# Optimization experiments

Measured on AMD Instinct MI355X. Metric: run time of the kernel, lower is better.

The kernel has to match this reference:

```python
import jax, jax.numpy as jnp
import numpy as np

P = 16; D = 256; NH = 8; L = 4; E = 8; K = 2; B = 32; IMG = 224; NC = 1000; FF = 4 * D
N = (IMG // P) ** 2  # 196 patches
HD = D // NH  # head dim
EPS = 1e-5


def setup_inputs():
    key = jax.random.key(0)
    ks = iter(jax.random.split(key, 16))
    s = 0.02  # init scale keeps softmax/logits well-conditioned
    rn = lambda shape: jax.random.normal(next(ks), shape, jnp.float32) * s
    return dict(
        x=jax.random.normal(next(ks), (B, 3, IMG, IMG), jnp.float32),
        patch_w=rn((3 * P * P, D)), patch_b=jnp.zeros((D,), jnp.float32),
        cls_token=rn((1, 1, D)), pos_embed=rn((1, N + 1, D)),
        router_w=rn((L, D, E)), router_b=jnp.zeros((L, E), jnp.float32),
        ln1_g=jnp.ones((L, E, D), jnp.float32), ln1_b=jnp.zeros((L, E, D), jnp.float32),
        qkv_w=rn((L, E, D, 3 * D)), qkv_b=jnp.zeros((L, E, 3 * D), jnp.float32),
        proj_w=rn((L, E, D, D)), proj_b=jnp.zeros((L, E, D), jnp.float32),
        ln2_g=jnp.ones((L, E, D), jnp.float32), ln2_b=jnp.zeros((L, E, D), jnp.float32),
        fc1_w=rn((L, E, D, FF)), fc1_b=jnp.zeros((L, E, FF), jnp.float32),
        fc2_w=rn((L, E, FF, D)), fc2_b=jnp.zeros((L, E, D), jnp.float32),
        norm_g=jnp.ones((D,), jnp.float32), norm_b=jnp.zeros((D,), jnp.float32),
        head_w=rn((D, NC)), head_b=jnp.zeros((NC,), jnp.float32),
    )


def _ln(x, g, b):
    m = x.mean(-1, keepdims=True)
    v = ((x - m) ** 2).mean(-1, keepdims=True)
    return (x - m) * jax.lax.rsqrt(v + EPS) * g + b


def _block(x, g1, b1, wqkv, bqkv, wp, bp, g2, b2, w1, bias1, w2, bias2):
    # standard ViT block: LN -> MHA -> residual, LN -> MLP(GELU) -> residual
    bsz, S, _ = x.shape
    h = _ln(x, g1, b1)
    qkv = (h @ wqkv + bqkv).reshape(bsz, S, 3, NH, HD)
    q, k, v = qkv[:, :, 0], qkv[:, :, 1], qkv[:, :, 2]  # [B,S,NH,HD]
    scores = jnp.einsum('bqhd,bkhd->bhqk', q, k) / np.float32(np.sqrt(HD))
    attn = jax.nn.softmax(scores, axis=-1)
    o = jnp.einsum('bhqk,bkhd->bqhd', attn, v).reshape(bsz, S, D)
    x = x + o @ wp + bp
    h2 = _ln(x, g2, b2)
    x = x + jax.nn.gelu(h2 @ w1 + bias1, approximate=False) @ w2 + bias2
    return x


def _moe_layer(x, rw, rb, g1, b1, wqkv, bqkv, wp, bp, g2, b2, w1, bias1, w2, bias2):
    probs = jax.nn.softmax(x @ rw + rb, axis=-1)            # [B,S,E]
    topv, topi = jax.lax.top_k(probs, K)                    # [B,S,K]
    topv = topv / topv.sum(-1, keepdims=True)
    # dense all-expert compute (faithful to source), vmapped over experts
    eo = jax.vmap(_block, in_axes=(None,) + (0,) * 12)(
        x, g1, b1, wqkv, bqkv, wp, bp, g2, b2, w1, bias1, w2, bias2)  # [E,B,S,D]
    eo = jnp.moveaxis(eo, 0, 2)                             # [B,S,E,D]
    sel = jnp.take_along_axis(eo, topi[..., None], axis=2)  # [B,S,K,D]
    return (sel * topv[..., None]).sum(axis=2)


def reference(x, patch_w, patch_b, cls_token, pos_embed, router_w, router_b,
              ln1_g, ln1_b, qkv_w, qkv_b, proj_w, proj_b, ln2_g, ln2_b,
              fc1_w, fc1_b, fc2_w, fc2_b, norm_g, norm_b, head_w, head_b):
    bsz = x.shape[0]
    g = IMG // P
    # patch embed: stride==kernel conv == patch extraction + matmul
    patches = x.reshape(bsz, 3, g, P, g, P).transpose(0, 2, 4, 1, 3, 5).reshape(bsz, N, 3 * P * P)
    h = patches @ patch_w + patch_b                          # [B,N,D]
    cls = jnp.broadcast_to(cls_token, (bsz, 1, D))
    h = jnp.concatenate([cls, h], axis=1) + pos_embed        # [B,N+1,D]
    for l in range(L):
        h = _moe_layer(h, router_w[l], router_b[l], ln1_g[l], ln1_b[l],
                       qkv_w[l], qkv_b[l], proj_w[l], proj_b[l], ln2_g[l], ln2_b[l],
                       fc1_w[l], fc1_b[l], fc2_w[l], fc2_b[l])
    h = _ln(h, norm_g, norm_b)
    return h[:, 0] @ head_w + head_b                         # [B,NC]
```

## Files before the change

kernel.cpp:

```cpp
#include <hip/hip_runtime.h>
#include <math.h>

#define SEQ 197
#define BATCH 32
#define DIM 256
#define NHEAD 8
#define HDIM 32
#define NEXP 8
#define NLAYER 4
#define FFDIM 1024
#define NCLS 1000
#define NPATCH 196
#define TOK (BATCH * SEQ)
#define CAP 13120
#define YB 99
#define YB128 50
#define KT 64

__device__ __forceinline__ void gload16(const float* g, float* l) {
  __builtin_amdgcn_global_load_lds(
      (const __attribute__((address_space(1))) void*)g,
      (__attribute__((address_space(3))) void*)l, 16, 0, 0);
}

__global__ __launch_bounds__(256) void k_im2col(const float* __restrict__ x,
                                                float* __restrict__ Apat) {
  int idx = blockIdx.x * 256 + threadIdx.x;
  if (idx >= BATCH * NPATCH * 768) return;
  int cpp = idx % 768;
  int m = idx / 768;
  int n = m % NPATCH;
  int b = m / NPATCH;
  int c = cpp >> 8;
  int py = (cpp >> 4) & 15;
  int px = cpp & 15;
  int gy = n / 14, gx = n % 14;
  Apat[idx] = x[(((size_t)b * 3 + c) * 224 + gy * 16 + py) * 224 + gx * 16 + px];
}

__global__ __launch_bounds__(256) void k_foldw(const float* __restrict__ qw,
                                               const float* __restrict__ g1,
                                               float* __restrict__ w4) {
  size_t idx = (size_t)blockIdx.x * 256 + threadIdx.x;
  if (idx >= (size_t)32 * 256 * 768) return;
  size_t kn = idx % (256 * 768);
  int le = (int)(idx / (256 * 768));
  int k = (int)(kn / 768);
  w4[idx] = qw[idx] * g1[le * 256 + k];
}

__global__ __launch_bounds__(256) void k_foldb(const float* __restrict__ qw,
                                               const float* __restrict__ qb,
                                               const float* __restrict__ b1,
                                               float* __restrict__ b4) {
  int le = blockIdx.y;
  int col = blockIdx.x * 256 + threadIdx.x;
  const float* w = qw + (size_t)le * 256 * 768 + col;
  const float* lb = b1 + (size_t)le * 256;
  float acc = 0.f;
  for (int k = 0; k < 256; ++k) acc = fmaf(lb[k], w[(size_t)k * 768], acc);
  b4[(size_t)le * 768 + col] = acc + qb[(size_t)le * 768 + col];
}

__global__ __launch_bounds__(256) void k_gemm_t(
    const float* __restrict__ A, const float* __restrict__ W,
    const float* __restrict__ bias, const float* __restrict__ R,
    const float* __restrict__ X2, const float* __restrict__ PW,
    const int* __restrict__ ptok, const int* __restrict__ off_e,
    const int* __restrict__ cnt_e, float* __restrict__ out, int M, int N,
    int K, int Ktot, int ksplit, int Wld, int wcol, int bstride, int ebase,
    int mode, int flags) {
  __shared__ float As[2][16][68];
  __shared__ float Bs[2][16][64];
  int gx = gridDim.x, gy = gridDim.y;
  int nwg = gx * gy * gridDim.z;
  int lin = blockIdx.x + gx * (blockIdx.y + gy * blockIdx.z);
  int q8 = nwg >> 3, r8 = nwg & 7;
  int xcd = lin & 7, jj0 = lin >> 3;
  int nlin = (xcd < r8 ? xcd * (q8 + 1) : r8 * (q8 + 1) + (xcd - r8) * q8) + jj0;
  int bx = nlin % gx;
  int t1 = nlin / gx;
  int by = t1 % gy;
  int bzf = t1 / gy;
  int kz = bzf % ksplit;
  int ez = bzf / ksplit;

  int e = ebase + ez;
  bool seg = (flags & 1) != 0;
  bool first = (kz == 0);
  int rows = seg ? cnt_e[e] : M;
  int row0 = by * 64;
  if (row0 >= rows) return;
  int col0 = bx * 64;
  int kbase = kz * K;
  int tid = threadIdx.x;
  int base = seg ? off_e[e] : 0;
  const float* Wp = W + (size_t)e * Ktot * Wld + wcol;
  const float* bp = bias + (size_t)e * bstride + wcol;

  int rr = tid >> 2, kq = (tid & 3) * 4;
  int r = row0 + rr;
  bool val = r < rows;
  int rc = val ? r : rows - 1;
  int gr0 = base + rc;
  int arow = seg ? ((flags & 2) ? ptok[gr0] : gr0) : rc;
  const float* aptr = A + (size_t)arow * Ktot + kbase + kq;
  float msk = val ? 1.f : 0.f;
  int wv = tid >> 6, lane = tid & 63;
  const float* bsrc = Wp + (size_t)(kbase + 4 * wv + (lane >> 4)) * Wld +
                      col0 + (lane & 15) * 4;

  gload16(bsrc, &Bs[0][4 * wv][0]);
  {
    float4 av = *(const float4*)aptr;
    As[0][kq + 0][rr] = av.x * msk;
    As[0][kq + 1][rr] = av.y * msk;
    As[0][kq + 2][rr] = av.z * msk;
    As[0][kq + 3][rr] = av.w * msk;
  }
  __syncthreads();

  int tx = tid & 15, ty = tid >> 4;
  float acc[4][4] = {};
  int cur = 0;
  for (int k0 = 0; k0 < K; k0 += 16) {
    int nb = cur ^ 1;
    bool more = (k0 + 16) < K;
    float4 av;
    if (more) {
      av = *(const float4*)(aptr + k0 + 16);
      gload16(bsrc + (size_t)(k0 + 16) * Wld, &Bs[nb][4 * wv][0]);
    }
#pragma unroll
    for (int k = 0; k < 16; ++k) {
      float4 a = *(const float4*)&As[cur][k][ty * 4];
      float4 b = *(const float4*)&Bs[cur][k][tx * 4];
      float aa[4] = {a.x, a.y, a.z, a.w};
      float bb[4] = {b.x, b.y, b.z, b.w};
#pragma unroll
      for (int i = 0; i < 4; ++i)
#pragma unroll
        for (int j = 0; j < 4; ++j) acc[i][j] = fmaf(aa[i], bb[j], acc[i][j]);
    }
    if (more) {
      As[nb][kq + 0][rr] = av.x * msk;
      As[nb][kq + 1][rr] = av.y * msk;
      As[nb][kq + 2][rr] = av.z * msk;
      As[nb][kq + 3][rr] = av.w * msk;
    }
    __syncthreads();
    cur = nb;
  }
#pragma unroll
  for (int i = 0; i < 4; ++i) {
    int rrow = row0 + ty * 4 + i;
    if (rrow >= rows) continue;
    int gr = base + rrow;
#pragma unroll
    for (int j = 0; j < 4; ++j) {
      int col = col0 + tx * 4 + j;
      float v = acc[i][j] + (first ? bp[col] : 0.f);
      if (mode == 0) {
        size_t orow = seg ? (size_t)gr : (size_t)bzf * M + rrow;
        out[orow * N + col] = v;
      } else if (mode == 1) {
        int t = ptok[gr];
        out[(size_t)gr * N + col] = v + R[(size_t)t * N + col];
      } else if (mode == 2) {
        out[(size_t)gr * N + col] =
            0.5f * v * (1.f + erff(v * 0.70710678118654752f));
      } else {
        int t = ptok[gr];
        float x2v = first ? X2[(size_t)gr * N + col] : 0.f;
        atomicAdd(&out[(size_t)t * N + col], PW[gr] * (x2v + v));
      }
    }
  }
}

__global__ __launch_bounds__(256) void k_gemm16(
    const float* __restrict__ A, const float* __restrict__ W,
    const float* __restrict__ bias, const float* __restrict__ R,
    const float* __restrict__ X2, const float* __restrict__ PW,
    const int* __restrict__ ptok, const int* __restrict__ off_e,
    const int* __restrict__ cnt_e, float* __restrict__ out, int M, int N,
    int K, int Wld, int wcol, int bstride, int ebase, int mode, int flags) {
  __shared__ float As[2][128][16];
  __shared__ float Bs[2][16][128];
  int gx = gridDim.x, gy = gridDim.y;
  int nwg = gx * gy * gridDim.z;
  int lin = blockIdx.x + gx * (blockIdx.y + gy * blockIdx.z);
  int q8 = nwg >> 3, r8 = nwg & 7;
  int xcd = lin & 7, jj0 = lin >> 3;
  int nlin = (xcd < r8 ? xcd * (q8 + 1) : r8 * (q8 + 1) + (xcd - r8) * q8) + jj0;
  int bx = nlin % gx;
  int t1 = nlin / gx;
  int by = t1 % gy;
  int bz = t1 / gy;

  int e = ebase + bz;
  bool seg = (flags & 1) != 0;
  int rows = seg ? cnt_e[e] : M;
  int row0 = by * 128;
  if (row0 >= rows) return;
  int col0 = bx * 128;
  int tid = threadIdx.x;
  int wv = tid >> 6, lane = tid & 63;
  int base = seg ? off_e[e] : 0;
  const float* Wp = W + (size_t)e * K * Wld + wcol;
  const float* bp = bias + (size_t)e * bstride + wcol;

  const float* pA0;
  const float* pA1;
  {
    int l4 = lane >> 2, lk = (lane & 3) * 4;
#pragma unroll
    for (int c = 0; c < 2; ++c) {
      int r = row0 + wv * 32 + c * 16 + l4;
      int rc = r < rows ? r : rows - 1;
      int gr0 = base + rc;
      int arow = seg ? ((flags & 2) ? ptok[gr0] : gr0) : rc;
      const float* p = A + (size_t)arow * K + lk;
      if (c == 0) pA0 = p; else pA1 = p;
    }
  }
  const float* pB = Wp + (size_t)(4 * wv + (lane >> 5)) * Wld + col0 +
                    (lane & 31) * 4;

  gload16(pA0, &As[0][wv * 32][0]);
  gload16(pA1, &As[0][wv * 32 + 16][0]);
  gload16(pB, &Bs[0][4 * wv][0]);
  gload16(pB + (size_t)2 * Wld, &Bs[0][4 * wv + 2][0]);
  __syncthreads();

  int tx = tid & 15, ty = tid >> 4;
  float acc0[8][4] = {};
  float acc1[8][4] = {};
  int cur = 0;
  for (int k0 = 0; k0 < K; k0 += 16) {
    int nb = cur ^ 1;
    bool more = (k0 + 16) < K;
    if (more) {
      gload16(pA0 + k0 + 16, &As[nb][wv * 32][0]);
      gload16(pA1 + k0 + 16, &As[nb][wv * 32 + 16][0]);
      gload16(pB + (size_t)(k0 + 16) * Wld, &Bs[nb][4 * wv][0]);
      gload16(pB + (size_t)(k0 + 18) * Wld, &Bs[nb][4 * wv + 2][0]);
    }
#pragma unroll
    for (int k4 = 0; k4 < 4; ++k4) {
      float a[8][4];
#pragma unroll
      for (int i = 0; i < 8; ++i) {
        float4 t = *(const float4*)&As[cur][ty + 16 * i][k4 * 4];
        a[i][0] = t.x;
        a[i][1] = t.y;
        a[i][2] = t.z;
        a[i][3] = t.w;
      }
#pragma unroll
      for (int kk = 0; kk < 4; ++kk) {
        float4 b0 = *(const float4*)&Bs[cur][k4 * 4 + kk][tx * 4];
        float4 b1 = *(const float4*)&Bs[cur][k4 * 4 + kk][64 + tx * 4];
        float b0a[4] = {b0.x, b0.y, b0.z, b0.w};
        float b1a[4] = {b1.x, b1.y, b1.z, b1.w};
#pragma unroll
        for (int i = 0; i < 8; ++i) {
          float av = a[i][kk];
#pragma unroll
          for (int j = 0; j < 4; ++j) {
            acc0[i][j] = fmaf(av, b0a[j], acc0[i][j]);
            acc1[i][j] = fmaf(av, b1a[j], acc1[i][j]);
          }
        }
      }
    }
    __syncthreads();
    cur = nb;
  }
#pragma unroll
  for (int i = 0; i < 8; ++i) {
    int rrow = row0 + ty + 16 * i;
    if (rrow >= rows) continue;
    int gr = base + rrow;
#pragma unroll
    for (int c = 0; c < 2; ++c) {
#pragma unroll
      for (int j = 0; j < 4; ++j) {
        int col = col0 + c * 64 + tx * 4 + j;
        float v = (c ? acc1[i][j] : acc0[i][j]) + bp[col];
        if (mode == 0) {
          size_t orow = seg ? (size_t)gr : (size_t)bz * M + rrow;
          out[orow * N + col] = v;
        } else if (mode == 1) {
          int t = ptok[gr];
          out[(size_t)gr * N + col] = v + R[(size_t)t * N + col];
        } else if (mode == 2) {
          out[(size_t)gr * N + col] =
              0.5f * v * (1.f + erff(v * 0.70710678118654752f));
        } else {
          int t = ptok[gr];
          atomicAdd(&out[(size_t)t * N + col],
                    PW[gr] * (X2[(size_t)gr * N + col] + v));
        }
      }
    }
  }
}

__global__ __launch_bounds__(256) void k_assemble(const float* __restrict__ tmp,
                                                  const float* __restrict__ cls,
                                                  const float* __restrict__ pos,
                                                  float* __restrict__ h) {
  int idx = blockIdx.x * 256 + threadIdx.x;
  if (idx >= TOK * DIM) return;
  int d = idx & 255;
  int t = idx >> 8;
  int s = t % SEQ;
  int b = t / SEQ;
  float v = (s == 0) ? cls[d] : tmp[((size_t)b * NPATCH + s - 1) * DIM + d];
  h[idx] = v + pos[s * DIM + d];
}

__global__ __launch_bounds__(64) void k_router(
    const float* __restrict__ h, const float* __restrict__ rw,
    const float* __restrict__ rb, int* __restrict__ cnt_eb,
    int* __restrict__ tmp_s, float* __restrict__ tmp_w) {
  int t = blockIdx.x;
  int lane = threadIdx.x;
  float hv[4];
  const float* hp = h + (size_t)t * DIM + lane * 4;
#pragma unroll
  for (int i = 0; i < 4; i++) hv[i] = hp[i];
  float lg[8];
#pragma unroll
  for (int e = 0; e < 8; e++) {
    float p = 0.f;
#pragma unroll
    for (int i = 0; i < 4; i++) p = fmaf(hv[i], rw[(lane * 4 + i) * 8 + e], p);
#pragma unroll
    for (int off = 32; off; off >>= 1) p += __shfl_down(p, off);
    lg[e] = p;
  }
  if (lane == 0) {
#pragma unroll
    for (int e = 0; e < 8; e++) lg[e] += rb[e];
    float mx = lg[0];
#pragma unroll
    for (int e = 1; e < 8; e++) mx = fmaxf(mx, lg[e]);
    float pr[8];
#pragma unroll
    for (int e = 0; e < 8; e++) pr[e] = expf(lg[e] - mx);
    int i0 = 0;
#pragma unroll
    for (int e = 1; e < 8; e++)
      if (pr[e] > pr[i0]) i0 = e;
    int i1 = -1;
#pragma unroll
    for (int e = 0; e < 8; e++)
      if (e != i0 && (i1 < 0 || pr[e] > pr[i1])) i1 = e;
    float wsum = pr[i0] + pr[i1];
    int b = t / SEQ, s = t - b * SEQ;
    int eb0 = i0 * 32 + b;
    int p0 = atomicAdd(&cnt_eb[eb0], 1);
    tmp_s[eb0 * SEQ + p0] = s;
    tmp_w[eb0 * SEQ + p0] = pr[i0] / wsum;
    int eb1 = i1 * 32 + b;
    int p1 = atomicAdd(&cnt_eb[eb1], 1);
    tmp_s[eb1 * SEQ + p1] = s;
    tmp_w[eb1 * SEQ + p1] = pr[i1] / wsum;
  }
}

__global__ __launch_bounds__(64) void k_scan(const int* __restrict__ cnt_eb,
                                             int* __restrict__ off_eb,
                                             int* __restrict__ off_e,
                                             int* __restrict__ cnt_e) {
  if (threadIdx.x == 0 && blockIdx.x == 0) {
    int g = 0;
    for (int e = 0; e < 8; e++) {
      off_e[e] = g;
      int ce = 0;
      for (int b = 0; b < 32; b++) {
        off_eb[e * 32 + b] = g + ce;
        ce += cnt_eb[e * 32 + b];
      }
      cnt_e[e] = ce;
      g += (ce + 63) & ~63;
    }
  }
}

__global__ __launch_bounds__(256) void k_scatter(
    const int* __restrict__ cnt_eb, const int* __restrict__ off_eb,
    const int* __restrict__ tmp_s, const float* __restrict__ tmp_w,
    int* __restrict__ ptok, float* __restrict__ pw) {
  int eb = blockIdx.x;
  int b = eb & 31;
  int c = cnt_eb[eb];
  int o = off_eb[eb];
  for (int i = threadIdx.x; i < c; i += 256) {
    ptok[o + i] = b * SEQ + tmp_s[eb * SEQ + i];
    pw[o + i] = tmp_w[eb * SEQ + i];
  }
}

__global__ __launch_bounds__(256) void k_ln_noaff(const float* __restrict__ X,
                                                  float* __restrict__ Y) {
  int t = blockIdx.x;
  int d = threadIdx.x;
  float v = X[(size_t)t * DIM + d];
  __shared__ float red[4];
  float s = v;
#pragma unroll
  for (int o = 32; o; o >>= 1) s += __shfl_down(s, o);
  if ((d & 63) == 0) red[d >> 6] = s;
  __syncthreads();
  float mean = (red[0] + red[1] + red[2] + red[3]) * (1.f / 256.f);
  __syncthreads();
  float c = v - mean;
  float s2 = c * c;
#pragma unroll
  for (int o = 32; o; o >>= 1) s2 += __shfl_down(s2, o);
  if ((d & 63) == 0) red[d >> 6] = s2;
  __syncthreads();
  float var = (red[0] + red[1] + red[2] + red[3]) * (1.f / 256.f);
  Y[(size_t)t * DIM + d] = c * rsqrtf(var + 1e-5f);
}

__global__ __launch_bounds__(256) void k_ln_seg(
    const float* __restrict__ X, const float* __restrict__ g,
    const float* __restrict__ bta, float* __restrict__ Y,
    const int* __restrict__ off_e, const int* __restrict__ cnt_e) {
  int e = blockIdx.y;
  int cnt = cnt_e[e];
  int base = off_e[e];
  int d = threadIdx.x;
  float gv = g[e * DIM + d];
  float bv = bta[e * DIM + d];
  __shared__ float red[4];
  for (int r = blockIdx.x; r < cnt; r += gridDim.x) {
    size_t gr = (size_t)(base + r);
    float v = X[gr * DIM + d];
    float s = v;
#pragma unroll
    for (int o = 32; o; o >>= 1) s += __shfl_down(s, o);
    if ((d & 63) == 0) red[d >> 6] = s;
    __syncthreads();
    float mean = (red[0] + red[1] + red[2] + red[3]) * (1.f / 256.f);
    __syncthreads();
    float c = v - mean;
    float s2 = c * c;
#pragma unroll
    for (int o = 32; o; o >>= 1) s2 += __shfl_down(s2, o);
    if ((d & 63) == 0) red[d >> 6] = s2;
    __syncthreads();
    float var = (red[0] + red[1] + red[2] + red[3]) * (1.f / 256.f);
    Y[gr * DIM + d] = c * rsqrtf(var + 1e-5f) * gv + bv;
    __syncthreads();
  }
}

__global__ __launch_bounds__(256) void k_attn(
    const float* __restrict__ qc, const float* __restrict__ kv,
    float* __restrict__ oc, const int* __restrict__ cnt_eb,
    const int* __restrict__ off_eb, int ebase) {
  int bx = blockIdx.x;
  int hh = bx & 7;
  int b = (bx >> 3) & 31;
  int ez = bx >> 8;
  int eb = (ebase + ez) * 32 + b;
  int cnt = cnt_eb[eb];
  if (cnt == 0) return;
  int off = off_eb[eb];
  __shared__ float Ks[KT][HDIM];
  __shared__ float Vs[KT][HDIM];
  const float* base = kv + ((size_t)ez * TOK + (size_t)b * SEQ) * 512;
  int tid = threadIdx.x;
  int grp = tid >> 2;
  int ln = tid & 3;
  int nrounds = (cnt + 63) >> 6;
  for (int qr = 0; qr < nrounds; ++qr) {
    int qi = qr * 64 + grp;
    bool act = qi < cnt;
    int qc_i = act ? qi : cnt - 1;
    const float* qp = qc + (size_t)(off + qc_i) * DIM + hh * HDIM + ln * 8;
    float4 q0 = *(const float4*)qp;
    float4 q1 = *(const float4*)(qp + 4);
    float qv[8] = {q0.x, q0.y, q0.z, q0.w, q1.x, q1.y, q1.z, q1.w};
    float m = -1e30f, l = 0.f;
    float acc[8] = {};
    for (int t0 = 0; t0 < SEQ; t0 += KT) {
      int nk = (SEQ - t0) < KT ? (SEQ - t0) : KT;
      __syncthreads();
      for (int i = tid; i < nk * 16; i += 256) {
        int row = i >> 4, half = (i >> 3) & 1, c4 = (i & 7) * 4;
        const float* p =
            base + (size_t)(t0 + row) * 512 + half * 256 + hh * HDIM + c4;
        if (half == 0)
          *(float4*)&Ks[row][c4] = *(const float4*)p;
        else
          *(float4*)&Vs[row][c4] = *(const float4*)p;
      }
      __syncthreads();
      const float* KsL = &Ks[0][ln * 8];
      const float* VsL = &Vs[0][ln * 8];
#pragma unroll 2
      for (int j = 0; j < nk; ++j) {
        const float4* kr = (const float4*)(KsL + j * HDIM);
        float4 k0 = kr[0], k1 = kr[1];
        float s = qv[0] * k0.x;
        s = fmaf(qv[1], k0.y, s);
        s = fmaf(qv[2], k0.z, s);
        s = fmaf(qv[3], k0.w, s);
        s = fmaf(qv[4], k1.x, s);
        s = fmaf(qv[5], k1.y, s);
        s = fmaf(qv[6], k1.z, s);
        s = fmaf(qv[7], k1.w, s);
        s += __shfl_xor(s, 1);
        s += __shfl_xor(s, 2);
        s *= 0.17677669529663687f;
        float nm = fmaxf(m, s);
        float f = expf(m - nm);
        float e2 = expf(s - nm);
        m = nm;
        l = fmaf(l, f, e2);
        const float4* vr = (const float4*)(VsL + j * HDIM);
        float4 v0 = vr[0], v1 = vr[1];
        acc[0] = fmaf(acc[0], f, e2 * v0.x);
        acc[1] = fmaf(acc[1], f, e2 * v0.y);
        acc[2] = fmaf(acc[2], f, e2 * v0.z);
        acc[3] = fmaf(acc[3], f, e2 * v0.w);
        acc[4] = fmaf(acc[4], f, e2 * v1.x);
        acc[5] = fmaf(acc[5], f, e2 * v1.y);
        acc[6] = fmaf(acc[6], f, e2 * v1.z);
        acc[7] = fmaf(acc[7], f, e2 * v1.w);
      }
    }
    if (act) {
      float inv = 1.f / l;
      float* op = oc + (size_t)(off + qi) * DIM + hh * HDIM + ln * 8;
      float4 o0 = {acc[0] * inv, acc[1] * inv, acc[2] * inv, acc[3] * inv};
      float4 o1 = {acc[4] * inv, acc[5] * inv, acc[6] * inv, acc[7] * inv};
      *(float4*)op = o0;
      *(float4*)(op + 4) = o1;
    }
  }
}

__global__ __launch_bounds__(256) void k_head(const float* __restrict__ h,
                                              const float* __restrict__ ng,
                                              const float* __restrict__ nb,
                                              const float* __restrict__ hw,
                                              const float* __restrict__ hb,
                                              float* __restrict__ out) {
  int b = blockIdx.x;
  int d = threadIdx.x;
  float v = h[(size_t)b * SEQ * DIM + d];
  __shared__ float red[4];
  __shared__ float hls[DIM];
  float s = v;
#pragma unroll
  for (int off = 32; off; off >>= 1) s += __shfl_down(s, off);
  if ((d & 63) == 0) red[d >> 6] = s;
  __syncthreads();
  float mean = (red[0] + red[1] + red[2] + red[3]) * (1.f / 256.f);
  __syncthreads();
  float c = v - mean;
  float s2 = c * c;
#pragma unroll
  for (int off = 32; off; off >>= 1) s2 += __shfl_down(s2, off);
  if ((d & 63) == 0) red[d >> 6] = s2;
  __syncthreads();
  float var = (red[0] + red[1] + red[2] + red[3]) * (1.f / 256.f);
  hls[d] = c * rsqrtf(var + 1e-5f) * ng[d] + nb[d];
  __syncthreads();
  for (int j = d; j < NCLS; j += 256) {
    float sdot = hb[j];
    for (int k2 = 0; k2 < DIM; k2++)
      sdot = fmaf(hls[k2], hw[(size_t)k2 * NCLS + j], sdot);
    out[(size_t)b * NCLS + j] = sdot;
  }
}

extern "C" void kernel_launch(void* const* d_in, const int* in_sizes, int n_in,
                              void* d_out, int out_size, void* d_ws,
                              size_t ws_size, hipStream_t stream) {
  const float* x = (const float*)d_in[0];
  const float* patch_w = (const float*)d_in[1];
  const float* patch_b = (const float*)d_in[2];
  const float* cls_token = (const float*)d_in[3];
  const float* pos_embed = (const float*)d_in[4];
  const float* router_w = (const float*)d_in[5];
  const float* router_b = (const float*)d_in[6];
  const float* ln1_g = (const float*)d_in[7];
  const float* ln1_b = (const float*)d_in[8];
  const float* qkv_w = (const float*)d_in[9];
  const float* qkv_b = (const float*)d_in[10];
  const float* proj_w = (const float*)d_in[11];
  const float* proj_b = (const float*)d_in[12];
  const float* ln2_g = (const float*)d_in[13];
  const float* ln2_b = (const float*)d_in[14];
  const float* fc1_w = (const float*)d_in[15];
  const float* fc1_b = (const float*)d_in[16];
  const float* fc2_w = (const float*)d_in[17];
  const float* fc2_b = (const float*)d_in[18];
  const float* norm_g = (const float*)d_in[19];
  const float* norm_b = (const float*)d_in[20];
  const float* head_w = (const float*)d_in[21];
  const float* head_b = (const float*)d_in[22];

  float* ws = (float*)d_ws;
  size_t off = 0;
  float* xhat = ws + off; off += (size_t)TOK * DIM;
  float* hbuf = ws + off; off += (size_t)TOK * DIM;
  float* accb = ws + off; off += (size_t)TOK * DIM;
  float* qc   = ws + off; off += (size_t)CAP * DIM;
  float* oc   = ws + off; off += (size_t)CAP * DIM;
  float* x2c  = ws + off; off += (size_t)CAP * DIM;
  float* ffc  = ws + off; off += (size_t)CAP * FFDIM;
  float* w4   = ws + off; off += (size_t)32 * DIM * 768;
  float* b4   = ws + off; off += (size_t)32 * 768;
  float* pwb  = ws + off; off += CAP;
  float* tmpw = ws + off; off += 256 * SEQ;
  int* ptok   = (int*)(ws + off); off += CAP;
  int* tmps   = (int*)(ws + off); off += 256 * SEQ;
  int* cnt_eb = (int*)(ws + off); off += 256;
  int* off_eb = (int*)(ws + off); off += 256;
  int* off_e  = (int*)(ws + off); off += 8;
  int* cnt_e  = (int*)(ws + off); off += 8;
  float* kv4 = ffc;
  float* hlnc = qc;

  k_foldw<<<(32 * 256 * 768 + 255) / 256, 256, 0, stream>>>(qkv_w, ln1_g, w4);
  k_foldb<<<dim3(3, 32), 256, 0, stream>>>(qkv_w, qkv_b, ln1_b, b4);

  int tot = BATCH * NPATCH * 768;
  k_im2col<<<(tot + 255) / 256, 256, 0, stream>>>(x, ffc);
  k_gemm_t<<<dim3(4, 98, 1), 256, 0, stream>>>(
      ffc, patch_w, patch_b, nullptr, nullptr, nullptr, nullptr, nullptr,
      nullptr, qc, BATCH * NPATCH, DIM, 768, 768, 1, DIM, 0, 0, 0, 0, 0);
  k_assemble<<<(TOK * DIM + 255) / 256, 256, 0, stream>>>(qc, cls_token,
                                                          pos_embed, hbuf);

  float* h = hbuf;
  float* acc = accb;
  for (int l = 0; l < NLAYER; ++l) {
    hipMemsetAsync(acc, 0, (size_t)TOK * DIM * sizeof(float), stream);
    hipMemsetAsync(cnt_eb, 0, 256 * sizeof(int), stream);
    k_router<<<TOK, 64, 0, stream>>>(h, router_w + (size_t)l * DIM * NEXP,
                                     router_b + (size_t)l * NEXP, cnt_eb, tmps,
                                     tmpw);
    k_scan<<<1, 64, 0, stream>>>(cnt_eb, off_eb, off_e, cnt_e);
    k_scatter<<<256, 256, 0, stream>>>(cnt_eb, off_eb, tmps, tmpw, ptok, pwb);
    k_ln_noaff<<<TOK, 256, 0, stream>>>(h, xhat);

    const float* Wl = w4 + (size_t)l * NEXP * DIM * 768;
    const float* Bl = b4 + (size_t)l * NEXP * 768;

    k_gemm_t<<<dim3(4, YB, 8), 256, 0, stream>>>(
        xhat, Wl, Bl, nullptr, nullptr, nullptr, ptok, off_e, cnt_e, qc, 0,
        DIM, DIM, DIM, 1, 768, 0, 768, 0, 0, 3);

    for (int grp = 0; grp < 2; ++grp) {
      int eb0 = grp * 4;
      k_gemm16<<<dim3(4, YB128, 4), 256, 0, stream>>>(
          xhat, Wl, Bl, nullptr, nullptr, nullptr, nullptr, nullptr, nullptr,
          kv4, TOK, 512, DIM, 768, 256, 768, eb0, 0, 0);
      k_attn<<<1024, 256, 0, stream>>>(qc, kv4, oc, cnt_eb, off_eb, eb0);
    }

    k_gemm_t<<<dim3(4, YB, 8), 256, 0, stream>>>(
        oc, proj_w + (size_t)l * NEXP * DIM * DIM,
        proj_b + (size_t)l * NEXP * DIM, h, nullptr, nullptr, ptok, off_e,
        cnt_e, x2c, 0, DIM, DIM, DIM, 1, DIM, 0, DIM, 0, 1, 1);
    k_ln_seg<<<dim3(YB, 8), 256, 0, stream>>>(
        x2c, ln2_g + (size_t)l * NEXP * DIM, ln2_b + (size_t)l * NEXP * DIM,
        hlnc, off_e, cnt_e);
    k_gemm16<<<dim3(8, YB128, 8), 256, 0, stream>>>(
        hlnc, fc1_w + (size_t)l * NEXP * DIM * FFDIM,
        fc1_b + (size_t)l * NEXP * FFDIM, nullptr, nullptr, nullptr, ptok,
        off_e, cnt_e, ffc, 0, FFDIM, DIM, FFDIM, 0, FFDIM, 0, 2, 1);
    k_gemm_t<<<dim3(4, YB, 16), 256, 0, stream>>>(
        ffc, fc2_w + (size_t)l * NEXP * FFDIM * DIM,
        fc2_b + (size_t)l * NEXP * DIM, nullptr, x2c, pwb, ptok, off_e, cnt_e,
        acc, 0, DIM, 512, FFDIM, 2, DIM, 0, DIM, 0, 3, 1);
    float* t = h;
    h = acc;
    acc = t;
  }
  k_head<<<BATCH, 256, 0, stream>>>(h, norm_g, norm_b, head_w, head_b,
                                    (float*)d_out);
}
```

Measured before the change: 3.464 ms.

## Compute Q with dense K/V GEMM per expert pair and drop fc2 split-K

The separate segmented Q GEMM is removed. The dense per-expert GEMM now produces the full Q, K and V for every token, and attention gathers each routed token's Q by token index. Experts are processed in groups of two instead of four, which keeps the larger QKV buffer within the existing workspace. Split-K is removed from the fc2 GEMM, cutting atomic adds in half at the cost of less parallelism. Q is now computed for all tokens instead of only routed ones, which adds dense FLOPs and doubles the number of launches in the attention loop.

```diff
diff --git a/kernel.cpp b/kernel.cpp
--- a/kernel.cpp
+++ b/kernel.cpp
@@ -68,8 +68,7 @@
     const float* __restrict__ X2, const float* __restrict__ PW,
     const int* __restrict__ ptok, const int* __restrict__ off_e,
     const int* __restrict__ cnt_e, float* __restrict__ out, int M, int N,
-    int K, int Ktot, int ksplit, int Wld, int wcol, int bstride, int ebase,
-    int mode, int flags) {
+    int K, int Wld, int wcol, int bstride, int ebase, int mode, int flags) {
   __shared__ float As[2][16][68];
   __shared__ float Bs[2][16][64];
   int gx = gridDim.x, gy = gridDim.y;
@@ -81,21 +80,17 @@
   int bx = nlin % gx;
   int t1 = nlin / gx;
   int by = t1 % gy;
-  int bzf = t1 / gy;
-  int kz = bzf % ksplit;
-  int ez = bzf / ksplit;
+  int ez = t1 / gy;
 
   int e = ebase + ez;
   bool seg = (flags & 1) != 0;
-  bool first = (kz == 0);
   int rows = seg ? cnt_e[e] : M;
   int row0 = by * 64;
   if (row0 >= rows) return;
   int col0 = bx * 64;
-  int kbase = kz * K;
   int tid = threadIdx.x;
   int base = seg ? off_e[e] : 0;
-  const float* Wp = W + (size_t)e * Ktot * Wld + wcol;
+  const float* Wp = W + (size_t)e * K * Wld + wcol;
   const float* bp = bias + (size_t)e * bstride + wcol;
 
   int rr = tid >> 2, kq = (tid & 3) * 4;
@@ -104,11 +99,11 @@
   int rc = val ? r : rows - 1;
   int gr0 = base + rc;
   int arow = seg ? ((flags & 2) ? ptok[gr0] : gr0) : rc;
-  const float* aptr = A + (size_t)arow * Ktot + kbase + kq;
+  const float* aptr = A + (size_t)arow * K + kq;
   float msk = val ? 1.f : 0.f;
   int wv = tid >> 6, lane = tid & 63;
-  const float* bsrc = Wp + (size_t)(kbase + 4 * wv + (lane >> 4)) * Wld +
-                      col0 + (lane & 15) * 4;
+  const float* bsrc = Wp + (size_t)(4 * wv + (lane >> 4)) * Wld + col0 +
+                      (lane & 15) * 4;
 
   gload16(bsrc, &Bs[0][4 * wv][0]);
   {
@@ -159,9 +154,9 @@
 #pragma unroll
     for (int j = 0; j < 4; ++j) {
       int col = col0 + tx * 4 + j;
-      float v = acc[i][j] + (first ? bp[col] : 0.f);
+      float v = acc[i][j] + bp[col];
       if (mode == 0) {
-        size_t orow = seg ? (size_t)gr : (size_t)bzf * M + rrow;
+        size_t orow = seg ? (size_t)gr : (size_t)ez * M + rrow;
         out[orow * N + col] = v;
       } else if (mode == 1) {
         int t = ptok[gr];
@@ -171,8 +166,8 @@
             0.5f * v * (1.f + erff(v * 0.70710678118654752f));
       } else {
         int t = ptok[gr];
-        float x2v = first ? X2[(size_t)gr * N + col] : 0.f;
-        atomicAdd(&out[(size_t)t * N + col], PW[gr] * (x2v + v));
+        atomicAdd(&out[(size_t)t * N + col],
+                  PW[gr] * (X2[(size_t)gr * N + col] + v));
       }
     }
   }
@@ -461,9 +456,9 @@
 }
 
 __global__ __launch_bounds__(256) void k_attn(
-    const float* __restrict__ qc, const float* __restrict__ kv,
-    float* __restrict__ oc, const int* __restrict__ cnt_eb,
-    const int* __restrict__ off_eb, int ebase) {
+    const float* __restrict__ qkv, float* __restrict__ oc,
+    const int* __restrict__ cnt_eb, const int* __restrict__ off_eb,
+    const int* __restrict__ ptok, int ebase) {
   int bx = blockIdx.x;
   int hh = bx & 7;
   int b = (bx >> 3) & 31;
@@ -474,7 +469,8 @@
   int off = off_eb[eb];
   __shared__ float Ks[KT][HDIM];
   __shared__ float Vs[KT][HDIM];
-  const float* base = kv + ((size_t)ez * TOK + (size_t)b * SEQ) * 512;
+  const float* base = qkv + ((size_t)ez * TOK + (size_t)b * SEQ) * 768;
+  const float* qbase = qkv + (size_t)ez * TOK * 768;
   int tid = threadIdx.x;
   int grp = tid >> 2;
   int ln = tid & 3;
@@ -483,7 +479,8 @@
     int qi = qr * 64 + grp;
     bool act = qi < cnt;
     int qc_i = act ? qi : cnt - 1;
-    const float* qp = qc + (size_t)(off + qc_i) * DIM + hh * HDIM + ln * 8;
+    int tok = ptok[off + qc_i];
+    const float* qp = qbase + (size_t)tok * 768 + hh * HDIM + ln * 8;
     float4 q0 = *(const float4*)qp;
     float4 q1 = *(const float4*)(qp + 4);
     float qv[8] = {q0.x, q0.y, q0.z, q0.w, q1.x, q1.y, q1.z, q1.w};
@@ -494,8 +491,8 @@
       __syncthreads();
       for (int i = tid; i < nk * 16; i += 256) {
         int row = i >> 4, half = (i >> 3) & 1, c4 = (i & 7) * 4;
-        const float* p =
-            base + (size_t)(t0 + row) * 512 + half * 256 + hh * HDIM + c4;
+        const float* p = base + (size_t)(t0 + row) * 768 + 256 + half * 256 +
+                         hh * HDIM + c4;
         if (half == 0)
           *(float4*)&Ks[row][c4] = *(const float4*)p;
         else
@@ -628,7 +625,7 @@
   int* off_eb = (int*)(ws + off); off += 256;
   int* off_e  = (int*)(ws + off); off += 8;
   int* cnt_e  = (int*)(ws + off); off += 8;
-  float* kv4 = ffc;
+  float* qkv2 = ffc;
   float* hlnc = qc;
 
   k_foldw<<<(32 * 256 * 768 + 255) / 256, 256, 0, stream>>>(qkv_w, ln1_g, w4);
@@ -638,7 +635,7 @@
   k_im2col<<<(tot + 255) / 256, 256, 0, stream>>>(x, ffc);
   k_gemm_t<<<dim3(4, 98, 1), 256, 0, stream>>>(
       ffc, patch_w, patch_b, nullptr, nullptr, nullptr, nullptr, nullptr,
-      nullptr, qc, BATCH * NPATCH, DIM, 768, 768, 1, DIM, 0, 0, 0, 0, 0);
+      nullptr, qc, BATCH * NPATCH, DIM, 768, DIM, 0, 0, 0, 0, 0);
   k_assemble<<<(TOK * DIM + 255) / 256, 256, 0, stream>>>(qc, cls_token,
                                                           pos_embed, hbuf);
 
@@ -657,22 +654,18 @@
     const float* Wl = w4 + (size_t)l * NEXP * DIM * 768;
     const float* Bl = b4 + (size_t)l * NEXP * 768;
 
-    k_gemm_t<<<dim3(4, YB, 8), 256, 0, stream>>>(
-        xhat, Wl, Bl, nullptr, nullptr, nullptr, ptok, off_e, cnt_e, qc, 0,
-        DIM, DIM, DIM, 1, 768, 0, 768, 0, 0, 3);
-
-    for (int grp = 0; grp < 2; ++grp) {
-      int eb0 = grp * 4;
-      k_gemm16<<<dim3(4, YB128, 4), 256, 0, stream>>>(
+    for (int grp = 0; grp < 4; ++grp) {
+      int eb0 = grp * 2;
+      k_gemm16<<<dim3(6, YB128, 2), 256, 0, stream>>>(
           xhat, Wl, Bl, nullptr, nullptr, nullptr, nullptr, nullptr, nullptr,
-          kv4, TOK, 512, DIM, 768, 256, 768, eb0, 0, 0);
-      k_attn<<<1024, 256, 0, stream>>>(qc, kv4, oc, cnt_eb, off_eb, eb0);
+          qkv2, TOK, 768, DIM, 768, 0, 768, eb0, 0, 0);
+      k_attn<<<512, 256, 0, stream>>>(qkv2, oc, cnt_eb, off_eb, ptok, eb0);
     }
 
     k_gemm_t<<<dim3(4, YB, 8), 256, 0, stream>>>(
         oc, proj_w + (size_t)l * NEXP * DIM * DIM,
         proj_b + (size_t)l * NEXP * DIM, h, nullptr, nullptr, ptok, off_e,
-        cnt_e, x2c, 0, DIM, DIM, DIM, 1, DIM, 0, DIM, 0, 1, 1);
+        cnt_e, x2c, 0, DIM, DIM, DIM, 0, DIM, 0, 1, 1);
     k_ln_seg<<<dim3(YB, 8), 256, 0, stream>>>(
         x2c, ln2_g + (size_t)l * NEXP * DIM, ln2_b + (size_t)l * NEXP * DIM,
         hlnc, off_e, cnt_e);
@@ -680,10 +673,10 @@
         hlnc, fc1_w + (size_t)l * NEXP * DIM * FFDIM,
         fc1_b + (size_t)l * NEXP * FFDIM, nullptr, nullptr, nullptr, ptok,
         off_e, cnt_e, ffc, 0, FFDIM, DIM, FFDIM, 0, FFDIM, 0, 2, 1);
-    k_gemm_t<<<dim3(4, YB, 16), 256, 0, stream>>>(
+    k_gemm_t<<<dim3(4, YB, 8), 256, 0, stream>>>(
         ffc, fc2_w + (size_t)l * NEXP * FFDIM * DIM,
         fc2_b + (size_t)l * NEXP * DIM, nullptr, x2c, pwb, ptok, off_e, cnt_e,
-        acc, 0, DIM, 512, FFDIM, 2, DIM, 0, DIM, 0, 3, 1);
+        acc, 0, DIM, FFDIM, DIM, 0, DIM, 0, 3, 1);
     float* t = h;
     h = acc;
     acc = t;
```

After: 3.950 ms. 14.0% more time.
